# Kernel optimization log

Hardware: AMD Instinct MI355X
Metric: run time of the kernel (lower is better)

## Reference

```python
import jax, jax.numpy as jnp
import numpy as np

W_BITS = 8       # default precision = max(precisions)
MIN_PREC = 4     # min(precisions)
GROUP_SIZE = 128


def make_new_byte_indices(total_bytes: int) -> np.ndarray:
    # Replicates make_new_byte_indices_torch. Note: in the torch code,
    # argsort(argsort(new_idx)) == new_idx (it is a permutation), so the
    # "unpermute" is a gather with new_idx itself.
    bytes_per_thread = 4
    threads_per_warp = 32
    bytes_per_warp = threads_per_warp * bytes_per_thread  # 128
    full = total_bytes // bytes_per_warp * bytes_per_warp
    rem = total_bytes - full
    parts = []
    if full > 0:
        bi = np.arange(full)
        warp_offsets = (bi // bytes_per_warp) * bytes_per_warp
        thread_indices = bi % threads_per_warp
        byte_off = ((bi % bytes_per_warp) // threads_per_warp) ^ 3
        parts.append(warp_offsets + thread_indices * bytes_per_thread + byte_off)
    if rem > 0:
        ri = np.arange(rem)
        adj = rem // bytes_per_thread
        if adj > 0:
            warp_offsets = (ri // bytes_per_warp) * bytes_per_warp
            thread_indices = ri % adj
            byte_off = (ri // adj) ^ 3
            parts.append(warp_offsets + thread_indices * 4 + byte_off + full)
        else:
            parts.append(np.arange(full, full + rem))
    return np.concatenate(parts).astype(np.int64)


def dequant(qweight, scale, zero, w_bits=W_BITS):
    _, N, in_chunks = qweight.shape
    total_bytes = in_chunks * 4
    in_features = in_chunks * 32
    q = qweight[:w_bits]
    # little-endian byte view of int32 (matches torch .view(torch.uint8))
    b = jnp.stack([(q >> (8 * k)) & 0xFF for k in range(4)], axis=-1)
    b = b.reshape(w_bits, N, total_bytes)  # int32 values in [0,255]
    idx = jnp.asarray(make_new_byte_indices(total_bytes))
    b = b[:, :, idx]
    # unpack bits, MSB first within each byte
    bits = jnp.stack([(b >> i) & 1 for i in reversed(range(8))], axis=-1)
    bits = bits.reshape(w_bits, N, in_features)  # [w_bits, N, in_features]
    plane_w = jnp.asarray([1 << (w_bits - 1 - k) for k in range(w_bits)], dtype=jnp.int32)
    qw = jnp.einsum('b,bni->ni', plane_w, bits)  # int32 in [0, 2^w_bits-1]
    weight_f = qw.astype(jnp.float32)
    bit_err = w_bits - MIN_PREC
    zero = zero * (2.0 ** bit_err)
    scale_pc = jnp.repeat(scale, GROUP_SIZE, axis=1)[:, :in_features]
    zero_pc = jnp.repeat(zero, GROUP_SIZE, axis=1)[:, :in_features]
    return scale_pc * (weight_f - zero_pc)  # [N, in_features]


def setup_inputs() -> dict:
    key = jax.random.key(0)
    kx, kq, ks, kz, kb = jax.random.split(key, 5)
    B, S, IN, OUT, G = 4, 2048, 4096, 4096, GROUP_SIZE
    x = jax.random.normal(kx, (B, S, IN), dtype=jnp.float32)
    qweight = jax.random.randint(kq, (8, OUT, IN // 32), 0, 2147483647, dtype=jnp.int32)
    scale = jax.random.uniform(ks, (OUT, IN // G), dtype=jnp.float32) * 0.01 + 1e-4
    zero = jax.random.uniform(kz, (OUT, IN // G), dtype=jnp.float32) * 8.0
    bias = jax.random.normal(kb, (OUT,), dtype=jnp.float32)
    return {"x": x, "qweight": qweight, "scale": scale, "zero": zero, "bias": bias}


def reference(x, qweight, scale, zero, bias):
    weight = dequant(qweight, scale, zero, W_BITS)  # [out, in]
    return jnp.matmul(x, weight.T) + bias
```

## Files before the change

### kernel.cpp

```cpp
#include <hip/hip_runtime.h>
#include <hip/hip_bf16.h>
#include <stdint.h>

typedef __attribute__((ext_vector_type(8))) short short8;
typedef __attribute__((ext_vector_type(4))) float f32x4;

#define M_DIM 8192
#define N_DIM 4096
#define K_DIM 4096
#define BM 256
#define BN 256
#define BK 64

static __device__ __forceinline__ unsigned short f32_to_bf16(float f) {
  union { float f; unsigned int u; } v; v.f = f;
  unsigned int u = v.u;
  u += 0x7fffu + ((u >> 16) & 1u);
  return (unsigned short)(u >> 16);
}

__global__ void cast_x_kernel(const float* __restrict__ x,
                              unsigned short* __restrict__ xb) {
  size_t i = ((size_t)blockIdx.x * blockDim.x + threadIdx.x) * 8;
  if (i >= (size_t)M_DIM * K_DIM) return;
  float4 v0 = *reinterpret_cast<const float4*>(x + i);
  float4 v1 = *reinterpret_cast<const float4*>(x + i + 4);
  short8 o;
  o[0] = (short)f32_to_bf16(v0.x);
  o[1] = (short)f32_to_bf16(v0.y);
  o[2] = (short)f32_to_bf16(v0.z);
  o[3] = (short)f32_to_bf16(v0.w);
  o[4] = (short)f32_to_bf16(v1.x);
  o[5] = (short)f32_to_bf16(v1.y);
  o[6] = (short)f32_to_bf16(v1.z);
  o[7] = (short)f32_to_bf16(v1.w);
  *reinterpret_cast<short8*>(xb + i) = o;
}

__global__ void dequant_kernel(const int* __restrict__ qw,
                               const float* __restrict__ scale,
                               const float* __restrict__ zero,
                               unsigned short* __restrict__ W) {
  int idx = blockIdx.x * blockDim.x + threadIdx.x;
  if (idx >= N_DIM * 128) return;
  int n = idx >> 7;
  int c = idx & 127;
  unsigned int w[8];
#pragma unroll
  for (int k = 0; k < 8; ++k)
    w[k] = (unsigned int)qw[(size_t)k * (N_DIM * 128) + idx];
  int wp = c >> 5, t = c & 31;
#pragma unroll
  for (int s = 0; s < 4; ++s) {
    int r = s ^ 3;
    unsigned int by[8];
#pragma unroll
    for (int k = 0; k < 8; ++k) by[k] = (w[k] >> (8 * r)) & 0xffu;
    int ibase = wp * 1024 + s * 256 + t * 8;
    int g = ibase >> 7;
    float sc = scale[n * 32 + g];
    float zp = zero[n * 32 + g] * 16.0f;
    short8 o;
#pragma unroll
    for (int u = 0; u < 8; ++u) {
      unsigned int q = 0;
#pragma unroll
      for (int k = 0; k < 8; ++k)
        q |= ((by[k] >> (7 - u)) & 1u) << (7 - k);
      o[u] = (short)f32_to_bf16(sc * ((float)q - zp));
    }
    *reinterpret_cast<short8*>(&W[(size_t)n * K_DIM + ibase]) = o;
  }
}


#define VMCNT2 asm volatile("s_waitcnt vmcnt(2)" ::: "memory")
#define VMCNT0 asm volatile("s_waitcnt vmcnt(0)" ::: "memory")
#define NOOP ((void)0)

#define STG(G, GROWB, KT, LDSC) do {                                           \
  const unsigned short* sb_ = (G) + ((size_t)(GROWB) * K_DIM + (KT) * 64);     \
  __builtin_amdgcn_global_load_lds(                                            \
      (const __attribute__((address_space(1))) void*)(sb_ + s_off0),           \
      (__attribute__((address_space(3))) void*)(smem + (LDSC) + wslot),        \
      16, 0, 0);                                                               \
  __builtin_amdgcn_global_load_lds(                                            \
      (const __attribute__((address_space(1))) void*)(sb_ + s_off1),           \
      (__attribute__((address_space(3))) void*)(smem + (LDSC) + 8192 + wslot), \
      16, 0, 0);                                                               \
} while (0)
#define STG_A(BUF, H, KT) STG(Ag, m0 + (H)*128, (KT), ((BUF)*2 + (H)) * 16384)
#define STG_B(BUF, H, KT) STG(Bg, n0 + (H)*128, (KT), 65536 + ((BUF)*2 + (H)) * 16384)

#define LA(BUF, QM, KK) do {                                                   \
  _Pragma("unroll") for (int mf_ = 0; mf_ < 4; ++mf_)                          \
    a_[mf_][KK] = *(const short8*)(smem + ((KK) ? a_off1 : a_off0) +           \
        (((BUF)*2 + (QM)) * 16384 + mf_ * 2048));                              \
} while (0)
#define LB(BUF, QN, KK) do {                                                   \
  _Pragma("unroll") for (int nf_ = 0; nf_ < 2; ++nf_)                          \
    b_[nf_][KK] = *(const short8*)(smem + ((KK) ? b_off1 : b_off0) +           \
        (((BUF)*2 + (QN)) * 16384 + nf_ * 2048));                              \
} while (0)

#define MFMA_KK(QM, QN, KK)                                                    \
  _Pragma("unroll") for (int mf_ = 0; mf_ < 4; ++mf_)                          \
    _Pragma("unroll") for (int nf_ = 0; nf_ < 2; ++nf_)                        \
      acc[QM][QN][mf_][nf_] = __builtin_amdgcn_mfma_f32_16x16x32_bf16(         \
          a_[mf_][KK], b_[nf_][KK], acc[QM][QN][mf_][nf_], 0, 0, 0)

#define REGION(QM, QN, RD0, RD1, STAGE, WAITV) do {                            \
  __builtin_amdgcn_s_barrier();                                                \
  WAITV;                                                                       \
  __builtin_amdgcn_sched_barrier(0);                                           \
  __builtin_amdgcn_s_setprio(1);                                               \
  STAGE;                                                                       \
  MFMA_KK(QM, QN, 0);                                                          \
  RD0;                                                                         \
  __builtin_amdgcn_sched_barrier(0);                                           \
  MFMA_KK(QM, QN, 1);                                                          \
  RD1;                                                                         \
  __builtin_amdgcn_sched_barrier(0);                                           \
  __builtin_amdgcn_s_setprio(0);                                               \
} while (0)

__global__ __launch_bounds__(512, 2) void gemm_kernel(
    const unsigned short* __restrict__ Ag,
    const unsigned short* __restrict__ Bg,
    const float* __restrict__ bias,
    float* __restrict__ C) {
  __shared__ __align__(16) char smem[131072];

  int bid = blockIdx.x;
  int cpx = gridDim.x >> 3;
  int swz = (bid & 7) * cpx + (bid >> 3);
  int tm = swz >> 4;
  int tn = swz & 15;
  int m0 = tm * BM, n0 = tn * BN;

  int tid = threadIdx.x;
  int lane = tid & 63;
  int wid = tid >> 6;
  int wr = wid >> 2, wc = wid & 3;

  const int xorv = (lane & 7) << 4;
  const int hi4 = (lane >> 4) << 4;
  const int wrbase = wr * 64 + (lane & 15);
  const int wcbase = wc * 32 + (lane & 15);
  const int a_off0 = (wrbase << 7) + (hi4 ^ xorv);
  const int a_off1 = (wrbase << 7) + ((64 | hi4) ^ xorv);
  const int b_off0 = 65536 + (wcbase << 7) + (hi4 ^ xorv);
  const int b_off1 = 65536 + (wcbase << 7) + ((64 | hi4) ^ xorv);
  const int wslot = (tid >> 6) << 10;
  const int s_lr0 = tid >> 3, s_lr1 = 64 + (tid >> 3);
  const int s_off0 = s_lr0 * K_DIM + (((tid & 7) ^ (s_lr0 & 7)) << 3);
  const int s_off1 = s_lr1 * K_DIM + (((tid & 7) ^ (s_lr1 & 7)) << 3);

  short8 a_[4][2], b_[2][2];
  f32x4 acc[2][2][4][2];
#pragma unroll
  for (int i = 0; i < 2; ++i)
#pragma unroll
    for (int j = 0; j < 2; ++j)
#pragma unroll
      for (int mf = 0; mf < 4; ++mf)
#pragma unroll
        for (int nf = 0; nf < 2; ++nf) acc[i][j][mf][nf] = (f32x4){0.f, 0.f, 0.f, 0.f};

  STG_B(0, 0, 0); STG_A(0, 0, 0); STG_B(0, 1, 0); STG_A(0, 1, 0);
  STG_A(1, 0, 1);
  VMCNT2;
  __builtin_amdgcn_s_barrier();
  LA(0, 0, 0); LB(0, 0, 0); LA(0, 0, 1); LB(0, 0, 1);

  for (int t = 0; t < 31; ++t) {
    const int kt1 = 2 * t + 1;
    REGION(0, 0, LB(0,1,0),            LB(0,1,1),            STG_B(1,0,kt1),   VMCNT2);
    REGION(0, 1, LA(0,1,0),            LA(0,1,1),            STG_B(1,1,kt1),   VMCNT2);
    REGION(1, 1, LB(0,0,0),            LB(0,0,1),            STG_A(1,1,kt1),   VMCNT2);
    REGION(1, 0, LA(1,0,0); LB(1,0,0), LA(1,0,1); LB(1,0,1), STG_B(0,0,kt1+1), VMCNT2);
    REGION(0, 0, LB(1,1,0),            LB(1,1,1),            STG_A(0,0,kt1+1), VMCNT2);
    REGION(0, 1, LA(1,1,0),            LA(1,1,1),            STG_B(0,1,kt1+1), VMCNT2);
    REGION(1, 1, LB(1,0,0),            LB(1,0,1),            STG_A(0,1,kt1+1), VMCNT2);
    REGION(1, 0, LA(0,0,0); LB(0,0,0), LA(0,0,1); LB(0,0,1), STG_A(1,0,kt1+2), VMCNT2);
  }
  REGION(0, 0, LB(0,1,0),            LB(0,1,1),            STG_B(1,0,63), VMCNT2);
  REGION(0, 1, LA(0,1,0),            LA(0,1,1),            STG_B(1,1,63), VMCNT2);
  REGION(1, 1, LB(0,0,0),            LB(0,0,1),            STG_A(1,1,63), VMCNT2);
  REGION(1, 0, LA(1,0,0); LB(1,0,0), LA(1,0,1); LB(1,0,1), NOOP,          VMCNT2);
  REGION(0, 0, LB(1,1,0),            LB(1,1,1),            NOOP,          VMCNT0);
  REGION(0, 1, LA(1,1,0),            LA(1,1,1),            NOOP,          NOOP);
  REGION(1, 1, LB(1,0,0),            LB(1,0,1),            NOOP,          NOOP);
  REGION(1, 0, NOOP,                 NOOP,                 NOOP,          NOOP);

#pragma unroll
  for (int qn = 0; qn < 2; ++qn)
#pragma unroll
    for (int nf = 0; nf < 2; ++nf) {
      int gcol = n0 + qn * 128 + wc * 32 + nf * 16 + (lane & 15);
      float bv = bias[gcol];
#pragma unroll
      for (int qm = 0; qm < 2; ++qm)
#pragma unroll
        for (int mf = 0; mf < 4; ++mf) {
          int grow = m0 + qm * 128 + wr * 64 + mf * 16 + ((lane >> 4) << 2);
          f32x4 v = acc[qm][qn][mf][nf];
#pragma unroll
          for (int j = 0; j < 4; ++j)
            C[(size_t)(grow + j) * N_DIM + gcol] = v[j] + bv;
        }
    }
}

extern "C" void kernel_launch(void* const* d_in, const int* in_sizes, int n_in,
                              void* d_out, int out_size, void* d_ws, size_t ws_size,
                              hipStream_t stream) {
  const float* x       = (const float*)d_in[0];
  const int*   qweight = (const int*)d_in[1];
  const float* scale   = (const float*)d_in[2];
  const float* zero    = (const float*)d_in[3];
  const float* bias    = (const float*)d_in[4];
  float* out = (float*)d_out;

  unsigned short* Xb = (unsigned short*)d_ws;
  unsigned short* Wb = Xb + (size_t)M_DIM * K_DIM;

  cast_x_kernel<<<(M_DIM * K_DIM / 8) / 256, 256, 0, stream>>>(x, Xb);
  dequant_kernel<<<(N_DIM * 128) / 256, 256, 0, stream>>>(qweight, scale, zero, Wb);
  gemm_kernel<<<(M_DIM / BM) * (N_DIM / BN), 512, 0, stream>>>(Xb, Wb, bias, out);
}
```

Before: 263.1 us.

## Merge prep kernels and interleave LDS reads at finer MFMA granularity

The x cast and weight dequant kernels are merged into one launch that splits work by block index, saving one kernel launch and letting the two memory-bound phases overlap. Inside the GEMM, each region now issues MFMAs in four quarter-chunks with LDS fragment reads placed between them under sched_barriers, so LDS latency hides behind matrix ops. The extra scheduling barriers constrain the compiler and may raise register pressure or add stalls.

```diff
diff --git a/kernel.cpp b/kernel.cpp
--- a/kernel.cpp
+++ b/kernel.cpp
@@ -19,57 +19,56 @@
   return (unsigned short)(u >> 16);
 }
 
-__global__ void cast_x_kernel(const float* __restrict__ x,
-                              unsigned short* __restrict__ xb) {
-  size_t i = ((size_t)blockIdx.x * blockDim.x + threadIdx.x) * 8;
-  if (i >= (size_t)M_DIM * K_DIM) return;
-  float4 v0 = *reinterpret_cast<const float4*>(x + i);
-  float4 v1 = *reinterpret_cast<const float4*>(x + i + 4);
-  short8 o;
-  o[0] = (short)f32_to_bf16(v0.x);
-  o[1] = (short)f32_to_bf16(v0.y);
-  o[2] = (short)f32_to_bf16(v0.z);
-  o[3] = (short)f32_to_bf16(v0.w);
-  o[4] = (short)f32_to_bf16(v1.x);
-  o[5] = (short)f32_to_bf16(v1.y);
-  o[6] = (short)f32_to_bf16(v1.z);
-  o[7] = (short)f32_to_bf16(v1.w);
-  *reinterpret_cast<short8*>(xb + i) = o;
-}
-
-__global__ void dequant_kernel(const int* __restrict__ qw,
-                               const float* __restrict__ scale,
-                               const float* __restrict__ zero,
-                               unsigned short* __restrict__ W) {
-  int idx = blockIdx.x * blockDim.x + threadIdx.x;
-  if (idx >= N_DIM * 128) return;
-  int n = idx >> 7;
-  int c = idx & 127;
-  unsigned int w[8];
-#pragma unroll
-  for (int k = 0; k < 8; ++k)
-    w[k] = (unsigned int)qw[(size_t)k * (N_DIM * 128) + idx];
-  int wp = c >> 5, t = c & 31;
-#pragma unroll
-  for (int s = 0; s < 4; ++s) {
-    int r = s ^ 3;
-    unsigned int by[8];
-#pragma unroll
-    for (int k = 0; k < 8; ++k) by[k] = (w[k] >> (8 * r)) & 0xffu;
-    int ibase = wp * 1024 + s * 256 + t * 8;
-    int g = ibase >> 7;
-    float sc = scale[n * 32 + g];
-    float zp = zero[n * 32 + g] * 16.0f;
+__global__ void prep_kernel(const float* __restrict__ x,
+                            unsigned short* __restrict__ xb,
+                            const int* __restrict__ qw,
+                            const float* __restrict__ scale,
+                            const float* __restrict__ zero,
+                            unsigned short* __restrict__ W) {
+  if (blockIdx.x < 16384) {
+    size_t i = ((size_t)blockIdx.x * blockDim.x + threadIdx.x) * 8;
+    float4 v0 = *reinterpret_cast<const float4*>(x + i);
+    float4 v1 = *reinterpret_cast<const float4*>(x + i + 4);
     short8 o;
-#pragma unroll
-    for (int u = 0; u < 8; ++u) {
-      unsigned int q = 0;
-#pragma unroll
-      for (int k = 0; k < 8; ++k)
-        q |= ((by[k] >> (7 - u)) & 1u) << (7 - k);
-      o[u] = (short)f32_to_bf16(sc * ((float)q - zp));
+    o[0] = (short)f32_to_bf16(v0.x);
+    o[1] = (short)f32_to_bf16(v0.y);
+    o[2] = (short)f32_to_bf16(v0.z);
+    o[3] = (short)f32_to_bf16(v0.w);
+    o[4] = (short)f32_to_bf16(v1.x);
+    o[5] = (short)f32_to_bf16(v1.y);
+    o[6] = (short)f32_to_bf16(v1.z);
+    o[7] = (short)f32_to_bf16(v1.w);
+    *reinterpret_cast<short8*>(xb + i) = o;
+  } else {
+    int idx = (blockIdx.x - 16384) * blockDim.x + threadIdx.x;
+    int n = idx >> 7;
+    int c = idx & 127;
+    unsigned int w[8];
+#pragma unroll
+    for (int k = 0; k < 8; ++k)
+      w[k] = (unsigned int)qw[(size_t)k * (N_DIM * 128) + idx];
+    int wp = c >> 5, t = c & 31;
+#pragma unroll
+    for (int s = 0; s < 4; ++s) {
+      int r = s ^ 3;
+      unsigned int by[8];
+#pragma unroll
+      for (int k = 0; k < 8; ++k) by[k] = (w[k] >> (8 * r)) & 0xffu;
+      int ibase = wp * 1024 + s * 256 + t * 8;
+      int g = ibase >> 7;
+      float sc = scale[n * 32 + g];
+      float zp = zero[n * 32 + g] * 16.0f;
+      short8 o;
+#pragma unroll
+      for (int u = 0; u < 8; ++u) {
+        unsigned int q = 0;
+#pragma unroll
+        for (int k = 0; k < 8; ++k)
+          q |= ((by[k] >> (7 - u)) & 1u) << (7 - k);
+        o[u] = (short)f32_to_bf16(sc * ((float)q - zp));
+      }
+      *reinterpret_cast<short8*>(&W[(size_t)n * K_DIM + ibase]) = o;
     }
-    *reinterpret_cast<short8*>(&W[(size_t)n * K_DIM + ibase]) = o;
   }
 }
 
@@ -77,6 +76,7 @@
 #define VMCNT2 asm volatile("s_waitcnt vmcnt(2)" ::: "memory")
 #define VMCNT0 asm volatile("s_waitcnt vmcnt(0)" ::: "memory")
 #define NOOP ((void)0)
+#define SB0 __builtin_amdgcn_sched_barrier(0)
 
 #define STG(G, GROWB, KT, LDSC) do {                                           \
   const unsigned short* sb_ = (G) + ((size_t)(GROWB) * K_DIM + (KT) * 64);     \
@@ -92,8 +92,8 @@
 #define STG_A(BUF, H, KT) STG(Ag, m0 + (H)*128, (KT), ((BUF)*2 + (H)) * 16384)
 #define STG_B(BUF, H, KT) STG(Bg, n0 + (H)*128, (KT), 65536 + ((BUF)*2 + (H)) * 16384)
 
-#define LA(BUF, QM, KK) do {                                                   \
-  _Pragma("unroll") for (int mf_ = 0; mf_ < 4; ++mf_)                          \
+#define LA_H(BUF, QM, KK, M0) do {                                             \
+  _Pragma("unroll") for (int mf_ = M0; mf_ < (M0) + 2; ++mf_)                  \
     a_[mf_][KK] = *(const short8*)(smem + ((KK) ? a_off1 : a_off0) +           \
         (((BUF)*2 + (QM)) * 16384 + mf_ * 2048));                              \
 } while (0)
@@ -103,24 +103,23 @@
         (((BUF)*2 + (QN)) * 16384 + nf_ * 2048));                              \
 } while (0)
 
-#define MFMA_KK(QM, QN, KK)                                                    \
-  _Pragma("unroll") for (int mf_ = 0; mf_ < 4; ++mf_)                          \
+#define MFMA_Q(QM, QN, KK, M0)                                                 \
+  _Pragma("unroll") for (int mf_ = M0; mf_ < (M0) + 2; ++mf_)                  \
     _Pragma("unroll") for (int nf_ = 0; nf_ < 2; ++nf_)                        \
       acc[QM][QN][mf_][nf_] = __builtin_amdgcn_mfma_f32_16x16x32_bf16(         \
           a_[mf_][KK], b_[nf_][KK], acc[QM][QN][mf_][nf_], 0, 0, 0)
 
-#define REGION(QM, QN, RD0, RD1, STAGE, WAITV) do {                            \
+#define REGION(QM, QN, R1, R2, R3, R4, STAGE, WAITV) do {                      \
   __builtin_amdgcn_s_barrier();                                                \
   WAITV;                                                                       \
-  __builtin_amdgcn_sched_barrier(0);                                           \
+  SB0;                                                                         \
   __builtin_amdgcn_s_setprio(1);                                               \
   STAGE;                                                                       \
-  MFMA_KK(QM, QN, 0);                                                          \
-  RD0;                                                                         \
-  __builtin_amdgcn_sched_barrier(0);                                           \
-  MFMA_KK(QM, QN, 1);                                                          \
-  RD1;                                                                         \
-  __builtin_amdgcn_sched_barrier(0);                                           \
+  SB0;                                                                         \
+  MFMA_Q(QM, QN, 0, 0); SB0; R1; SB0;                                          \
+  MFMA_Q(QM, QN, 0, 2); SB0; R2; SB0;                                          \
+  MFMA_Q(QM, QN, 1, 0); SB0; R3; SB0;                                          \
+  MFMA_Q(QM, QN, 1, 2); SB0; R4; SB0;                                          \
   __builtin_amdgcn_s_setprio(0);                                               \
 } while (0)
 
@@ -171,27 +170,28 @@
   STG_A(1, 0, 1);
   VMCNT2;
   __builtin_amdgcn_s_barrier();
-  LA(0, 0, 0); LB(0, 0, 0); LA(0, 0, 1); LB(0, 0, 1);
+  LA_H(0, 0, 0, 0); LA_H(0, 0, 0, 2); LB(0, 0, 0);
+  LA_H(0, 0, 1, 0); LA_H(0, 0, 1, 2); LB(0, 0, 1);
 
   for (int t = 0; t < 31; ++t) {
     const int kt1 = 2 * t + 1;
-    REGION(0, 0, LB(0,1,0),            LB(0,1,1),            STG_B(1,0,kt1),   VMCNT2);
-    REGION(0, 1, LA(0,1,0),            LA(0,1,1),            STG_B(1,1,kt1),   VMCNT2);
-    REGION(1, 1, LB(0,0,0),            LB(0,0,1),            STG_A(1,1,kt1),   VMCNT2);
-    REGION(1, 0, LA(1,0,0); LB(1,0,0), LA(1,0,1); LB(1,0,1), STG_B(0,0,kt1+1), VMCNT2);
-    REGION(0, 0, LB(1,1,0),            LB(1,1,1),            STG_A(0,0,kt1+1), VMCNT2);
-    REGION(0, 1, LA(1,1,0),            LA(1,1,1),            STG_B(0,1,kt1+1), VMCNT2);
-    REGION(1, 1, LB(1,0,0),            LB(1,0,1),            STG_A(0,1,kt1+1), VMCNT2);
-    REGION(1, 0, LA(0,0,0); LB(0,0,0), LA(0,0,1); LB(0,0,1), STG_A(1,0,kt1+2), VMCNT2);
+    REGION(0, 0, NOOP,            LB(0,1,0),                  NOOP,            LB(0,1,1),                  STG_B(1,0,kt1),   VMCNT2);
+    REGION(0, 1, LA_H(0,1,0,0),   LA_H(0,1,0,2),              LA_H(0,1,1,0),   LA_H(0,1,1,2),              STG_B(1,1,kt1),   VMCNT2);
+    REGION(1, 1, NOOP,            LB(0,0,0),                  NOOP,            LB(0,0,1),                  STG_A(1,1,kt1),   VMCNT2);
+    REGION(1, 0, LA_H(1,0,0,0),   LA_H(1,0,0,2); LB(1,0,0),   LA_H(1,0,1,0),   LA_H(1,0,1,2); LB(1,0,1),   STG_B(0,0,kt1+1), VMCNT2);
+    REGION(0, 0, NOOP,            LB(1,1,0),                  NOOP,            LB(1,1,1),                  STG_A(0,0,kt1+1), VMCNT2);
+    REGION(0, 1, LA_H(1,1,0,0),   LA_H(1,1,0,2),              LA_H(1,1,1,0),   LA_H(1,1,1,2),              STG_B(0,1,kt1+1), VMCNT2);
+    REGION(1, 1, NOOP,            LB(1,0,0),                  NOOP,            LB(1,0,1),                  STG_A(0,1,kt1+1), VMCNT2);
+    REGION(1, 0, LA_H(0,0,0,0),   LA_H(0,0,0,2); LB(0,0,0),   LA_H(0,0,1,0),   LA_H(0,0,1,2); LB(0,0,1),   STG_A(1,0,kt1+2), VMCNT2);
   }
-  REGION(0, 0, LB(0,1,0),            LB(0,1,1),            STG_B(1,0,63), VMCNT2);
-  REGION(0, 1, LA(0,1,0),            LA(0,1,1),            STG_B(1,1,63), VMCNT2);
-  REGION(1, 1, LB(0,0,0),            LB(0,0,1),            STG_A(1,1,63), VMCNT2);
-  REGION(1, 0, LA(1,0,0); LB(1,0,0), LA(1,0,1); LB(1,0,1), NOOP,          VMCNT2);
-  REGION(0, 0, LB(1,1,0),            LB(1,1,1),            NOOP,          VMCNT0);
-  REGION(0, 1, LA(1,1,0),            LA(1,1,1),            NOOP,          NOOP);
-  REGION(1, 1, LB(1,0,0),            LB(1,0,1),            NOOP,          NOOP);
-  REGION(1, 0, NOOP,                 NOOP,                 NOOP,          NOOP);
+  REGION(0, 0, NOOP,            LB(0,1,0),                  NOOP,            LB(0,1,1),                  STG_B(1,0,63), VMCNT2);
+  REGION(0, 1, LA_H(0,1,0,0),   LA_H(0,1,0,2),              LA_H(0,1,1,0),   LA_H(0,1,1,2),              STG_B(1,1,63), VMCNT2);
+  REGION(1, 1, NOOP,            LB(0,0,0),                  NOOP,            LB(0,0,1),                  STG_A(1,1,63), VMCNT2);
+  REGION(1, 0, LA_H(1,0,0,0),   LA_H(1,0,0,2); LB(1,0,0),   LA_H(1,0,1,0),   LA_H(1,0,1,2); LB(1,0,1),   NOOP,          VMCNT2);
+  REGION(0, 0, NOOP,            LB(1,1,0),                  NOOP,            LB(1,1,1),                  NOOP,          VMCNT0);
+  REGION(0, 1, LA_H(1,1,0,0),   LA_H(1,1,0,2),              LA_H(1,1,1,0),   LA_H(1,1,1,2),              NOOP,          NOOP);
+  REGION(1, 1, NOOP,            LB(1,0,0),                  NOOP,            LB(1,0,1),                  NOOP,          NOOP);
+  REGION(1, 0, NOOP,            NOOP,                       NOOP,            NOOP,                       NOOP,          NOOP);
 
 #pragma unroll
   for (int qn = 0; qn < 2; ++qn)
@@ -225,7 +225,6 @@
   unsigned short* Xb = (unsigned short*)d_ws;
   unsigned short* Wb = Xb + (size_t)M_DIM * K_DIM;
 
-  cast_x_kernel<<<(M_DIM * K_DIM / 8) / 256, 256, 0, stream>>>(x, Xb);
-  dequant_kernel<<<(N_DIM * 128) / 256, 256, 0, stream>>>(qweight, scale, zero, Wb);
+  prep_kernel<<<16384 + 2048, 256, 0, stream>>>(x, Xb, qweight, scale, zero, Wb);
   gemm_kernel<<<(M_DIM / BM) * (N_DIM / BN), 512, 0, stream>>>(Xb, Wb, bias, out);
 }
```

Result: no change. 263.6 us (+0.2%).
